# Performance work log

Measured on AMD Instinct MI355X. Metric: run time of the kernel, lower is better.

The kernel has to match this reference:

```python
import jax, jax.numpy as jnp
import numpy as np

N_NODES = 200000
N_GRAPHS = 4000


def _sage_conv(x, src, dst, W_l, b_l, W_r, num_nodes):
    # PyG SAGEConv (aggr='mean'): out = lin_l(mean_{j in N(i)} x_j) + lin_r(x_i)
    msg_sum = jax.ops.segment_sum(x[src], dst, num_segments=num_nodes)      # [N, d]
    deg = jax.ops.segment_sum(jnp.ones_like(src, dtype=x.dtype), dst,
                              num_segments=num_nodes)                       # [N]
    mean_nbr = msg_sum / jnp.maximum(deg, 1.0)[:, None]
    return mean_nbr @ W_l.T + b_l + x @ W_r.T


def setup_inputs() -> dict:
    key = jax.random.key(0)
    ks = jax.random.split(key, 10)
    in_ch, hid, out = 32, 64, 2
    E = 3200000
    x = jax.random.normal(ks[0], (N_NODES, in_ch), dtype=jnp.float32)
    edge_index = jax.random.randint(ks[1], (2, E), 0, N_NODES, dtype=jnp.int64)
    batch = jnp.sort(jax.random.randint(ks[2], (N_NODES,), 0, N_GRAPHS, dtype=jnp.int64))

    def glorot(k, shape):
        lim = 1.0 / np.sqrt(shape[1])
        return jax.random.uniform(k, shape, jnp.float32, -lim, lim)

    return {
        "x": x,
        "edge_index": edge_index,
        "batch": batch,
        "W1_l": glorot(ks[3], (hid, in_ch)),
        "b1": jnp.zeros((hid,), jnp.float32),
        "W1_r": glorot(ks[4], (hid, in_ch)),
        "W2_l": glorot(ks[5], (hid, hid)),
        "b2": jnp.zeros((hid,), jnp.float32),
        "W2_r": glorot(ks[6], (hid, hid)),
        "W_lin": glorot(ks[7], (out, hid)),
        "b_lin": jnp.zeros((out,), jnp.float32),
    }


def reference(x, edge_index, batch, W1_l, b1, W1_r, W2_l, b2, W2_r, W_lin, b_lin):
    src, dst = edge_index[0], edge_index[1]
    h = jax.nn.relu(_sage_conv(x, src, dst, W1_l, b1, W1_r, N_NODES))
    h = jax.nn.relu(_sage_conv(h, src, dst, W2_l, b2, W2_r, N_NODES))
    # global_mean_pool over graph ids
    pool_sum = jax.ops.segment_sum(h, batch, num_segments=N_GRAPHS)          # [G, 64]
    cnt = jax.ops.segment_sum(jnp.ones_like(batch, dtype=h.dtype), batch,
                              num_segments=N_GRAPHS)                          # [G]
    pooled = pool_sum / jnp.maximum(cnt, 1.0)[:, None]
    return pooled @ W_lin.T + b_lin
```

## Files before the change

### kernel.cpp

```cpp
#include <hip/hip_runtime.h>
#include <hip/hip_bf16.h>


#define WS_ALIGN 64
#define EPB 4096
#define BSHIFT 8
#define BNODES 256
#define BCAP 6144
#define MAXNB 1024

typedef short bf16x8 __attribute__((ext_vector_type(8)));
typedef float f32x4 __attribute__((ext_vector_type(4)));

__device__ inline unsigned short f2bf(float f) {
    unsigned u = __float_as_uint(f);
    return (unsigned short)((u + 0x7fffu + ((u >> 16) & 1u)) >> 16);
}

__device__ inline void acc8(const uint4 u, float* a) {
    a[0] += __uint_as_float(u.x << 16);
    a[1] += __uint_as_float(u.x & 0xffff0000u);
    a[2] += __uint_as_float(u.y << 16);
    a[3] += __uint_as_float(u.y & 0xffff0000u);
    a[4] += __uint_as_float(u.z << 16);
    a[5] += __uint_as_float(u.z & 0xffff0000u);
    a[6] += __uint_as_float(u.w << 16);
    a[7] += __uint_as_float(u.w & 0xffff0000u);
}


__global__ void prep_kernel(const float* __restrict__ x, unsigned short* __restrict__ xb,
                            const float* __restrict__ W1_l, const float* __restrict__ W1_r,
                            const float* __restrict__ W2_l, const float* __restrict__ W2_r,
                            unsigned short* __restrict__ whi1, unsigned short* __restrict__ whi2,
                            int* __restrict__ bucketCursor, float* __restrict__ pool,
                            int N, int NB, int G, int total4) {
    const int gid = blockIdx.x * blockDim.x + threadIdx.x;
    if (gid < total4) {
        const float4 v = reinterpret_cast<const float4*>(x)[gid];
        ushort4 o;
        o.x = f2bf(v.x); o.y = f2bf(v.y); o.z = f2bf(v.z); o.w = f2bf(v.w);
        reinterpret_cast<ushort4*>(xb)[gid] = o;
    }
    if (gid < NB) bucketCursor[gid] = gid * BCAP;
    if (gid < G * 64) pool[gid] = 0.0f;
    if (gid < 64 * 64) {
        const int o = gid >> 6, k = gid & 63;
        const float v = (k < 32) ? W1_l[o * 32 + k] : W1_r[o * 32 + (k - 32)];
        whi1[gid] = f2bf(v);
    }
    if (gid < 64 * 128) {
        const int o = gid >> 7, k = gid & 127;
        const float v = (k < 64) ? W2_l[o * 64 + k] : W2_r[o * 64 + (k - 64)];
        whi2[gid] = f2bf(v);
    }
}


__global__ __launch_bounds__(256) void bucket_scatter_kernel(const int* __restrict__ src,
                                                             const int* __restrict__ dst,
                                                             int* __restrict__ bucketCursor,
                                                             unsigned* __restrict__ bucketData,
                                                             int E, int NB) {
    __shared__ int hist[MAXNB];
    __shared__ int cur[MAXNB];
    const int t = threadIdx.x;
    for (int i = t; i < MAXNB; i += 256) hist[i] = 0;
    __syncthreads();
    const int eBase = blockIdx.x * EPB + t;
    int s[16], b[16], dl[16];
#pragma unroll
    for (int j = 0; j < 16; ++j) {
        int e = eBase + j * 256;
        if (e < E) {
            int d = dst[e];
            s[j]  = src[e];
            b[j]  = d >> BSHIFT;
            dl[j] = d & (BNODES - 1);
            atomicAdd(&hist[b[j]], 1);
        } else {
            b[j] = -1;
        }
    }
    __syncthreads();
    for (int bb = t; bb < NB; bb += 256)
        if (hist[bb] > 0) cur[bb] = atomicAdd(&bucketCursor[bb], hist[bb]);
    __syncthreads();
#pragma unroll
    for (int j = 0; j < 16; ++j) {
        if (b[j] >= 0) {
            int pos = atomicAdd(&cur[b[j]], 1);
            if (pos < (b[j] + 1) * BCAP)
                bucketData[pos] = ((unsigned)s[j] << BSHIFT) | (unsigned)dl[j];
        }
    }
}

__global__ __launch_bounds__(256) void csr_build_kernel(const unsigned* __restrict__ bucketData,
                                                        const int* __restrict__ bucketCursor,
                                                        int* __restrict__ offs,
                                                        int* __restrict__ offe,
                                                        int* __restrict__ csr_src,
                                                        int N) {
    __shared__ int cnt[BNODES];
    __shared__ int sscan[BNODES];
    __shared__ int cur[BNODES];
    const int t   = threadIdx.x;
    const int bkt = blockIdx.x;
    const int nodeBase = bkt << BSHIFT;
    const int regionBase = bkt * BCAP;
    const int count = min(bucketCursor[bkt] - regionBase, BCAP);
    cnt[t] = 0;
    __syncthreads();
    for (int k = regionBase + t; k < regionBase + count; k += 256)
        atomicAdd(&cnt[bucketData[k] & (BNODES - 1)], 1);
    __syncthreads();
    int v0 = cnt[t];
    sscan[t] = v0;
    __syncthreads();
    for (int off = 1; off < 256; off <<= 1) {
        int v = (t >= off) ? sscan[t - off] : 0;
        __syncthreads();
        sscan[t] += v;
        __syncthreads();
    }
    const int excl = sscan[t] - v0;
    cur[t] = excl;
    const int node = nodeBase + t;
    if (node < N) {
        offs[node] = regionBase + excl;
        offe[node] = regionBase + excl + v0;
    }
    __syncthreads();
    for (int k = regionBase + t; k < regionBase + count; k += 256) {
        const unsigned v = bucketData[k];
        const int d = (int)(v & (BNODES - 1));
        const int pos = regionBase + atomicAdd(&cur[d], 1);
        csr_src[pos] = (int)(v >> BSHIFT);
    }
}


template <int DIN, bool POOL>
__launch_bounds__(256)
__global__ void fused_agg_mfma_kernel(const unsigned short* __restrict__ featb,
                                      const unsigned short* __restrict__ whi,
                                      const float* __restrict__ bias,
                                      const int* __restrict__ csr_src,
                                      const int* __restrict__ offs,
                                      const int* __restrict__ offe,
                                      unsigned short* __restrict__ houtb,
                                      const int* __restrict__ batch,
                                      float* __restrict__ pool_sum,
                                      int N, int nSteps) {
    constexpr int K   = 2 * DIN;
    constexpr int STR = K + 8;
    constexpr int D8  = DIN / 8;
    constexpr int V   = DIN / 32;
    constexpr int EB  = 8 / V;
    __shared__ unsigned short A_s[64 * STR];
    const int tid = threadIdx.x;
    const int nodeBase = blockIdx.x * 64;

    for (int i = tid; i < 64 * D8; i += 256) {
        const int node = i / D8, q = i % D8;
        const int n = min(nodeBase + node, N - 1);
        const uint4 u = *reinterpret_cast<const uint4*>(featb + (size_t)n * DIN + q * 8);
        *reinterpret_cast<uint4*>(&A_s[node * STR + DIN + q * 8]) = u;
    }

    {
        const int node = tid >> 2;
        const int part = tid & 3;
        const int n = nodeBase + node;
        unsigned short* dp = &A_s[node * STR + part * (8 * V)];
        if (n < N) {
            const int beg = offs[n];
            const int end = offe[n];
            const uint4* base = reinterpret_cast<const uint4*>(featb);
            float a[8 * V];
#pragma unroll
            for (int i = 0; i < 8 * V; ++i) a[i] = 0.f;
            int k = beg;
            for (; k + EB <= end; k += EB) {
                int s[EB];
#pragma unroll
                for (int j = 0; j < EB; ++j) s[j] = csr_src[k + j];
                uint4 u[8];
#pragma unroll
                for (int j = 0; j < EB; ++j)
#pragma unroll
                    for (int v = 0; v < V; ++v)
                        u[j * V + v] = base[(size_t)s[j] * D8 + part * V + v];
#pragma unroll
                for (int j = 0; j < EB; ++j)
#pragma unroll
                    for (int v = 0; v < V; ++v)
                        acc8(u[j * V + v], &a[v * 8]);
            }
            for (; k + EB / 2 <= end; k += EB / 2) {
                int s[EB / 2];
#pragma unroll
                for (int j = 0; j < EB / 2; ++j) s[j] = csr_src[k + j];
                uint4 u[4];
#pragma unroll
                for (int j = 0; j < EB / 2; ++j)
#pragma unroll
                    for (int v = 0; v < V; ++v)
                        u[j * V + v] = base[(size_t)s[j] * D8 + part * V + v];
#pragma unroll
                for (int j = 0; j < EB / 2; ++j)
#pragma unroll
                    for (int v = 0; v < V; ++v)
                        acc8(u[j * V + v], &a[v * 8]);
            }
            for (; k < end; ++k) {
                const int s = csr_src[k];
#pragma unroll
                for (int v = 0; v < V; ++v) {
                    const uint4 u = base[(size_t)s * D8 + part * V + v];
                    acc8(u, &a[v * 8]);
                }
            }
            const float inv = 1.0f / fmaxf((float)(end - beg), 1.0f);
#pragma unroll
            for (int v = 0; v < V; ++v) {
                ushort4 lo, hi;
                lo.x = f2bf(a[v * 8 + 0] * inv); lo.y = f2bf(a[v * 8 + 1] * inv);
                lo.z = f2bf(a[v * 8 + 2] * inv); lo.w = f2bf(a[v * 8 + 3] * inv);
                hi.x = f2bf(a[v * 8 + 4] * inv); hi.y = f2bf(a[v * 8 + 5] * inv);
                hi.z = f2bf(a[v * 8 + 6] * inv); hi.w = f2bf(a[v * 8 + 7] * inv);
                *reinterpret_cast<ushort4*>(dp + v * 8)     = lo;
                *reinterpret_cast<ushort4*>(dp + v * 8 + 4) = hi;
            }
        } else {
            const ushort4 z = {0, 0, 0, 0};
#pragma unroll
            for (int v = 0; v < 2 * V; ++v)
                *reinterpret_cast<ushort4*>(dp + v * 4) = z;
        }
    }
    __syncthreads();

    const int lane = tid & 63;
    const int wave = tid >> 6;
    const int lr = lane & 15;
    const int q  = lane >> 4;
    f32x4 acc[4];
#pragma unroll
    for (int t = 0; t < 4; ++t) {
        const float b = bias[t * 16 + lr];
        acc[t] = (f32x4){b, b, b, b};
    }
    const unsigned short* Arow = &A_s[(wave * 16 + lr) * STR + q * 8];
    const unsigned short* Brow = whi + (size_t)lr * K + q * 8;
    for (int s = 0; s < nSteps; ++s) {
        const bf16x8 af = *reinterpret_cast<const bf16x8*>(Arow + s * 32);
#pragma unroll
        for (int t = 0; t < 4; ++t) {
            const bf16x8 bh = *reinterpret_cast<const bf16x8*>(
                Brow + (size_t)t * 16 * K + s * 32);
            acc[t] = __builtin_amdgcn_mfma_f32_16x16x32_bf16(af, bh, acc[t], 0, 0, 0);
        }
    }

    if (POOL) {
        float ag[4] = {0.f, 0.f, 0.f, 0.f};
        int gcur = -1;
        for (int reg = 0; reg < 4; ++reg) {
            const int n = nodeBase + wave * 16 + q * 4 + reg;
            if (n >= N) break;
            const int g = batch[n];
            if (g != gcur) {
                if (gcur >= 0) {
#pragma unroll
                    for (int t = 0; t < 4; ++t)
                        atomicAdd(&pool_sum[(size_t)gcur * 64 + t * 16 + lr], ag[t]);
                }
                gcur = g;
                ag[0] = ag[1] = ag[2] = ag[3] = 0.f;
            }
#pragma unroll
            for (int t = 0; t < 4; ++t)
                ag[t] += fmaxf(acc[t][reg], 0.0f);
        }
        if (gcur >= 0) {
#pragma unroll
            for (int t = 0; t < 4; ++t)
                atomicAdd(&pool_sum[(size_t)gcur * 64 + t * 16 + lr], ag[t]);
        }
    } else {
        for (int reg = 0; reg < 4; ++reg) {
            const int n = nodeBase + wave * 16 + q * 4 + reg;
            if (n >= N) break;
#pragma unroll
            for (int t = 0; t < 4; ++t)
                houtb[(size_t)n * 64 + t * 16 + lr] = f2bf(fmaxf(acc[t][reg], 0.0f));
        }
    }
}


__device__ inline int lower_bound_batch(const int* __restrict__ batch, int N, int key) {
    int lo = 0, hi = N;
    while (lo < hi) {
        const int mid = (lo + hi) >> 1;
        if (batch[mid] < key) lo = mid + 1; else hi = mid;
    }
    return lo;
}

__global__ void final_kernel(const float* __restrict__ pool_sum,
                             const int* __restrict__ batch,
                             const float* __restrict__ W_lin,
                             const float* __restrict__ b_lin,
                             float* __restrict__ out, int G, int N) {
    int t = blockIdx.x * blockDim.x + threadIdx.x;
    if (t >= G * 2) return;
    int g = t >> 1, o = t & 1;
    const int c0 = lower_bound_batch(batch, N, g);
    const int c1 = lower_bound_batch(batch, N, g + 1);
    float inv = 1.0f / fmaxf((float)(c1 - c0), 1.0f);
    float acc = b_lin[o];
#pragma unroll
    for (int c = 0; c < 64; ++c)
        acc = fmaf(pool_sum[(size_t)g * 64 + c] * inv, W_lin[o * 64 + c], acc);
    out[t] = acc;
}

extern "C" void kernel_launch(void* const* d_in, const int* in_sizes, int n_in,
                              void* d_out, int out_size, void* d_ws, size_t ws_size,
                              hipStream_t stream) {
    const float* x     = (const float*)d_in[0];
    const int*   ei    = (const int*)d_in[1];
    const int*   batch = (const int*)d_in[2];
    const float* W1_l  = (const float*)d_in[3];
    const float* b1    = (const float*)d_in[4];
    const float* W1_r  = (const float*)d_in[5];
    const float* W2_l  = (const float*)d_in[6];
    const float* b2    = (const float*)d_in[7];
    const float* W2_r  = (const float*)d_in[8];
    const float* W_lin = (const float*)d_in[9];
    const float* b_lin = (const float*)d_in[10];

    const int N = in_sizes[0] / 32;
    const int E = in_sizes[1] / 2;
    const int G = out_size / 2;
    const int* src = ei;
    const int* dst = ei + E;
    const int NB = (N + BNODES - 1) >> BSHIFT;

    char* p = (char*)d_ws;
    auto carve = [&](size_t bytes) -> void* {
        void* r = (void*)p;
        p += (bytes + (WS_ALIGN - 1)) / WS_ALIGN * WS_ALIGN;
        return r;
    };
    int*            bucketCursor = (int*)carve((size_t)MAXNB * 4);
    unsigned*       bucketData   = (unsigned*)carve((size_t)NB * BCAP * 4);
    int*            offs         = (int*)carve((size_t)N * 4);
    int*            offe         = (int*)carve((size_t)N * 4);
    int*            csr_src      = (int*)carve((size_t)NB * BCAP * 4);
    unsigned short* xb           = (unsigned short*)carve((size_t)N * 32 * 2);
    unsigned short* h1b          = (unsigned short*)carve((size_t)N * 64 * 2);
    unsigned short* whi1         = (unsigned short*)carve(64 * 64 * 2);
    unsigned short* whi2         = (unsigned short*)carve(64 * 128 * 2);
    float*          pool         = (float*)carve((size_t)G * 64 * 4);
    float*          out          = (float*)d_out;

    const int TB = 256;
    const int total4 = N * 32 / 4;
    prep_kernel<<<(total4 + TB - 1) / TB, TB, 0, stream>>>(
        x, xb, W1_l, W1_r, W2_l, W2_r, whi1, whi2, bucketCursor, pool,
        N, NB, G, total4);
    bucket_scatter_kernel<<<(E + EPB - 1) / EPB, TB, 0, stream>>>(src, dst, bucketCursor,
                                                                  bucketData, E, NB);
    csr_build_kernel<<<NB, TB, 0, stream>>>(bucketData, bucketCursor, offs, offe, csr_src, N);

    fused_agg_mfma_kernel<32, false><<<(N + 63) / 64, TB, 0, stream>>>(
        xb, whi1, b1, csr_src, offs, offe, h1b, nullptr, nullptr, N, 2);

    fused_agg_mfma_kernel<64, true><<<(N + 63) / 64, TB, 0, stream>>>(
        h1b, whi2, b2, csr_src, offs, offe, nullptr, batch, pool, N, 4);

    final_kernel<<<(G * 2 + TB - 1) / TB, TB, 0, stream>>>(pool, batch, W_lin, b_lin,
                                                           out, G, N);
}
```

Measured before the change: 358.6 us.

## Balance edge aggregation across threads with merge-path split and LDS atomics

Measured after the change: 416.5 us. +16.1%, slower.

```diff
diff --git a/kernel.cpp b/kernel.cpp
--- a/kernel.cpp
+++ b/kernel.cpp
@@ -153,12 +153,16 @@
                                       const int* __restrict__ batch,
                                       float* __restrict__ pool_sum,
                                       int N, int nSteps) {
-    constexpr int K   = 2 * DIN;
-    constexpr int STR = K + 8;
-    constexpr int D8  = DIN / 8;
-    constexpr int V   = DIN / 32;
-    constexpr int EB  = 8 / V;
+    constexpr int K    = 2 * DIN;
+    constexpr int STR  = K + 8;
+    constexpr int D8   = DIN / 8;
+    constexpr int V    = DIN / 32;
+    constexpr int EBATCH = 8 / V;
+    constexpr int ASTR = DIN + 1;
     __shared__ unsigned short A_s[64 * STR];
+    __shared__ float accS[64 * ASTR];
+    __shared__ int offsS[64];
+    __shared__ int offeS[64];
     const int tid = threadIdx.x;
     const int nodeBase = blockIdx.x * 64;
 
@@ -168,76 +172,108 @@
         const uint4 u = *reinterpret_cast<const uint4*>(featb + (size_t)n * DIN + q * 8);
         *reinterpret_cast<uint4*>(&A_s[node * STR + DIN + q * 8]) = u;
     }
+    for (int i = tid; i < 64 * ASTR; i += 256) accS[i] = 0.f;
+    if (tid < 64) {
+        const int n = nodeBase + tid;
+        const int nc = min(n, N - 1);
+        int s = offs[nc], e = offe[nc];
+        if (n >= N) s = e;
+        offsS[tid] = s;
+        offeS[tid] = e;
+    }
+    __syncthreads();
+
+    {
+        const int el = tid >> 2;
+        const int p  = tid & 3;
+        const int tileBeg = offsS[0];
+        const int tileEnd = offeS[63];
+        const int T = tileEnd - tileBeg;
+        const int chunk = (T + 63) >> 6;
+        int k    = tileBeg + el * chunk;
+        int kEnd = min(k + chunk, tileEnd);
+        if (k < kEnd) {
+            int lo = 0, hi = 63;
+            while (lo < hi) {
+                const int mid = (lo + hi) >> 1;
+                if (offeS[mid] <= k) lo = mid + 1; else hi = mid;
+            }
+            int node = lo;
+            int curEnd = offeS[node];
+            const uint4* base = reinterpret_cast<const uint4*>(featb);
+            float a[8 * V];
+#pragma unroll
+            for (int i = 0; i < 8 * V; ++i) a[i] = 0.f;
+
+            while (k + EBATCH <= kEnd) {
+                int sidx[EBATCH];
+#pragma unroll
+                for (int j = 0; j < EBATCH; ++j) sidx[j] = csr_src[k + j];
+                uint4 u[8];
+#pragma unroll
+                for (int j = 0; j < EBATCH; ++j)
+#pragma unroll
+                    for (int v = 0; v < V; ++v)
+                        u[j * V + v] = base[(size_t)sidx[j] * D8 + p * V + v];
+#pragma unroll
+                for (int j = 0; j < EBATCH; ++j) {
+                    while (k + j >= curEnd) {
+                        float* da = &accS[node * ASTR + p * (8 * V)];
+#pragma unroll
+                        for (int i = 0; i < 8 * V; ++i) {
+                            atomicAdd(&da[i], a[i]);
+                            a[i] = 0.f;
+                        }
+                        curEnd = offeS[++node];
+                    }
+#pragma unroll
+                    for (int v = 0; v < V; ++v) acc8(u[j * V + v], &a[v * 8]);
+                }
+                k += EBATCH;
+            }
+            while (k < kEnd) {
+                const int s0 = csr_src[k];
+                while (k >= curEnd) {
+                    float* da = &accS[node * ASTR + p * (8 * V)];
+#pragma unroll
+                    for (int i = 0; i < 8 * V; ++i) {
+                        atomicAdd(&da[i], a[i]);
+                        a[i] = 0.f;
+                    }
+                    curEnd = offeS[++node];
+                }
+#pragma unroll
+                for (int v = 0; v < V; ++v) {
+                    const uint4 u = base[(size_t)s0 * D8 + p * V + v];
+                    acc8(u, &a[v * 8]);
+                }
+                ++k;
+            }
+            {
+                float* da = &accS[node * ASTR + p * (8 * V)];
+#pragma unroll
+                for (int i = 0; i < 8 * V; ++i) atomicAdd(&da[i], a[i]);
+            }
+        }
+    }
+    __syncthreads();
 
     {
         const int node = tid >> 2;
-        const int part = tid & 3;
-        const int n = nodeBase + node;
-        unsigned short* dp = &A_s[node * STR + part * (8 * V)];
-        if (n < N) {
-            const int beg = offs[n];
-            const int end = offe[n];
-            const uint4* base = reinterpret_cast<const uint4*>(featb);
-            float a[8 * V];
-#pragma unroll
-            for (int i = 0; i < 8 * V; ++i) a[i] = 0.f;
-            int k = beg;
-            for (; k + EB <= end; k += EB) {
-                int s[EB];
-#pragma unroll
-                for (int j = 0; j < EB; ++j) s[j] = csr_src[k + j];
-                uint4 u[8];
-#pragma unroll
-                for (int j = 0; j < EB; ++j)
-#pragma unroll
-                    for (int v = 0; v < V; ++v)
-                        u[j * V + v] = base[(size_t)s[j] * D8 + part * V + v];
-#pragma unroll
-                for (int j = 0; j < EB; ++j)
-#pragma unroll
-                    for (int v = 0; v < V; ++v)
-                        acc8(u[j * V + v], &a[v * 8]);
-            }
-            for (; k + EB / 2 <= end; k += EB / 2) {
-                int s[EB / 2];
-#pragma unroll
-                for (int j = 0; j < EB / 2; ++j) s[j] = csr_src[k + j];
-                uint4 u[4];
-#pragma unroll
-                for (int j = 0; j < EB / 2; ++j)
-#pragma unroll
-                    for (int v = 0; v < V; ++v)
-                        u[j * V + v] = base[(size_t)s[j] * D8 + part * V + v];
-#pragma unroll
-                for (int j = 0; j < EB / 2; ++j)
-#pragma unroll
-                    for (int v = 0; v < V; ++v)
-                        acc8(u[j * V + v], &a[v * 8]);
-            }
-            for (; k < end; ++k) {
-                const int s = csr_src[k];
-#pragma unroll
-                for (int v = 0; v < V; ++v) {
-                    const uint4 u = base[(size_t)s * D8 + part * V + v];
-                    acc8(u, &a[v * 8]);
-                }
-            }
-            const float inv = 1.0f / fmaxf((float)(end - beg), 1.0f);
-#pragma unroll
-            for (int v = 0; v < V; ++v) {
-                ushort4 lo, hi;
-                lo.x = f2bf(a[v * 8 + 0] * inv); lo.y = f2bf(a[v * 8 + 1] * inv);
-                lo.z = f2bf(a[v * 8 + 2] * inv); lo.w = f2bf(a[v * 8 + 3] * inv);
-                hi.x = f2bf(a[v * 8 + 4] * inv); hi.y = f2bf(a[v * 8 + 5] * inv);
-                hi.z = f2bf(a[v * 8 + 6] * inv); hi.w = f2bf(a[v * 8 + 7] * inv);
-                *reinterpret_cast<ushort4*>(dp + v * 8)     = lo;
-                *reinterpret_cast<ushort4*>(dp + v * 8 + 4) = hi;
-            }
-        } else {
-            const ushort4 z = {0, 0, 0, 0};
-#pragma unroll
-            for (int v = 0; v < 2 * V; ++v)
-                *reinterpret_cast<ushort4*>(dp + v * 4) = z;
+        const int p = tid & 3;
+        const float deg = (float)(offeS[node] - offsS[node]);
+        const float inv = 1.0f / fmaxf(deg, 1.0f);
+        const float* sp = &accS[node * ASTR + p * (8 * V)];
+        unsigned short* dp = &A_s[node * STR + p * (8 * V)];
+#pragma unroll
+        for (int v = 0; v < V; ++v) {
+            ushort4 lo4, hi4;
+            lo4.x = f2bf(sp[v * 8 + 0] * inv); lo4.y = f2bf(sp[v * 8 + 1] * inv);
+            lo4.z = f2bf(sp[v * 8 + 2] * inv); lo4.w = f2bf(sp[v * 8 + 3] * inv);
+            hi4.x = f2bf(sp[v * 8 + 4] * inv); hi4.y = f2bf(sp[v * 8 + 5] * inv);
+            hi4.z = f2bf(sp[v * 8 + 6] * inv); hi4.w = f2bf(sp[v * 8 + 7] * inv);
+            *reinterpret_cast<ushort4*>(dp + v * 8)     = lo4;
+            *reinterpret_cast<ushort4*>(dp + v * 8 + 4) = hi4;
         }
     }
     __syncthreads();
```
